# Kernel optimization log

Measured on AMD Instinct MI355X. Metric: run time of the kernel, lower is better.

The kernel has to match this reference:

```python
import jax, jax.numpy as jnp
import numpy as np
import math

B, CZ, L = 1, 128, 256
H, C = 4, 32  # num_heads, head dim
EPS = 1e-5


def _conv1x1(w, x):
    # w: (out, in), x: (b, in, i, j) -> (b, out, i, j)
    return jnp.einsum('oc,bcij->boij', w, x)


def setup_inputs() -> dict:
    key = jax.random.key(0)
    ks = jax.random.split(key, 8)
    s = 1.0 / math.sqrt(CZ)
    return {
        'pair_rep': jax.random.normal(ks[0], (B, CZ, L, L), jnp.float32),
        'ln_gamma': jnp.ones((CZ, L, L), jnp.float32),
        'ln_beta': jnp.zeros((CZ, L, L), jnp.float32),
        'w_q': jax.random.normal(ks[1], (H * C, CZ), jnp.float32) * s,
        'w_k': jax.random.normal(ks[2], (H * C, CZ), jnp.float32) * s,
        'w_v': jax.random.normal(ks[3], (H * C, CZ), jnp.float32) * s,
        'w_b': jax.random.normal(ks[4], (H, CZ), jnp.float32) * s,
        'w_g': jax.random.normal(ks[5], (H * C, CZ), jnp.float32) * s,
        'b_g': jnp.zeros((H * C,), jnp.float32),
        'w_rep': jax.random.normal(ks[6], (CZ, H * C), jnp.float32) * s,
        'b_rep': jnp.zeros((CZ,), jnp.float32),
    }


def reference(pair_rep, ln_gamma, ln_beta, w_q, w_k, w_v, w_b, w_g, b_g, w_rep, b_rep):
    # LayerNorm over (c_z, h, w) jointly, full-shape affine (torch LayerNorm([c_z,h,w]))
    mu = jnp.mean(pair_rep, axis=(1, 2, 3), keepdims=True)
    var = jnp.var(pair_rep, axis=(1, 2, 3), keepdims=True)
    x = (pair_rep - mu) * jax.lax.rsqrt(var + EPS) * ln_gamma[None] + ln_beta[None]

    # 1x1 conv projections; channels packed as (h c): channel = h*C + c
    q = _conv1x1(w_q, x).reshape(B, H, C, L, L)  # bhcij
    k = _conv1x1(w_k, x).reshape(B, H, C, L, L)
    v = _conv1x1(w_v, x).reshape(B, H, C, L, L)
    bias = _conv1x1(w_b, x)                       # (b, h, i, j) -> used as bias[b,h,j,k]
    g = jax.nn.sigmoid(_conv1x1(w_g, x) + b_g[None, :, None, None]).reshape(B, H, C, L, L)

    scale = 1.0 / math.sqrt(C)
    # scores[b,h,i,j,k] = scale * sum_c q[b,h,c,i,j] k[b,h,c,i,k] + bias[b,h,j,k]
    scores = scale * jnp.einsum('bhcij,bhcik->bhijk', q, k) + bias[:, :, None, :, :]
    a = jax.nn.softmax(scores, axis=-1)
    # o[b,h,c,i,j] = sum_k a[b,h,i,j,k] v[b,h,c,i,k]  (same math as the 6D broadcast-sum)
    o = g * jnp.einsum('bhijk,bhcik->bhcij', a, v)

    # output repacks channels as (c h): channel = c*H + h
    o = jnp.transpose(o, (0, 2, 1, 3, 4)).reshape(B, C * H, L, L)
    return _conv1x1(w_rep, o) + b_rep[None, :, None, None]
```

## Files before the change

kernel.cpp:

```cpp
#include <hip/hip_runtime.h>
#include <math.h>

#define L 256
#define CZ 128
#define NH 4
#define HD 32
#define P (L*L)
#define NTOT (CZ*P)
#define EPSV 1e-5f
#define SCALE 0.17677669529663687f

typedef unsigned short u16;
typedef _Float16 f16;
typedef __attribute__((ext_vector_type(8))) _Float16 f16x8;
typedef __attribute__((ext_vector_type(4))) _Float16 f16x4;
typedef __attribute__((ext_vector_type(4))) float    f32x4;

__device__ __forceinline__ float bu2f(u16 u){ return __uint_as_float(((unsigned)u) << 16); }
__device__ __forceinline__ u16 f2bu(float x){
  unsigned u = __float_as_uint(x);
  return (u16)((u + 0x7fffu + ((u >> 16) & 1u)) >> 16);
}

__device__ __forceinline__ float ldr(bool fp32, const void* p, size_t i){
  return fp32 ? ((const float*)p)[i] : bu2f(((const u16*)p)[i]);
}
__device__ __forceinline__ void str(bool fp32, void* p, size_t i, float v){
  if (fp32) ((float*)p)[i] = v; else ((u16*)p)[i] = f2bu(v);
}
template<bool FP32>
__device__ __forceinline__ float ldin(const void* p, size_t i){
  return FP32 ? ((const float*)p)[i] : bu2f(((const u16*)p)[i]);
}
template<bool FP32>
__device__ __forceinline__ void stout(void* p, size_t i, float v){
  if (FP32) ((float*)p)[i] = v; else ((u16*)p)[i] = f2bu(v);
}

__device__ __forceinline__ void glds16(const void* g, void* l){
  __builtin_amdgcn_global_load_lds((const __attribute__((address_space(1))) void*)g,
                                   (__attribute__((address_space(3))) void*)l, 16, 0, 0);
}

#define OFF_WQT   16
#define OFF_WKT   (OFF_WQT+16384)
#define OFF_WVT   (OFF_WKT+16384)
#define OFF_WGT   (OFF_WVT+16384)
#define OFF_WREPT (OFF_WGT+16384)
#define OFF_WBT   (OFF_WREPT+16384)
#define OFF_BGF   (OFF_WBT+512)
#define OFF_BREPF (OFF_BGF+128)
#define OFF_BIAS  (OFF_BREPF+128)
#define OFF_XN    344848
#define OFF_ATTO  (OFF_XN+4194304)
#define WS_NEED   (((size_t)OFF_ATTO + 4194304ull)*4ull)

#define GUARD(ws) if (((((const volatile int*)(ws))[2]) != 0) != FP32) return;
#define RFLAG(ws) (((const volatile int*)(ws))[2] != 0)

__global__ __launch_bounds__(256) void detect_dtype(const void* pair, int* flag){
  int t = threadIdx.x;
  const u16* u = (const u16*)pair;
  int big = 0;
  for (int k = t; k < 2048; k += 256){
    float av = fabsf(bu2f(u[k]));
    if (!(av < 1e4f)) big = 1;
  }
  __shared__ int sb[256];
  sb[t] = big; __syncthreads();
  for (int off = 128; off > 0; off >>= 1){
    if (t < off) sb[t] |= sb[t+off];
    __syncthreads();
  }
  if (t == 0) flag[2] = sb[0];
}

__global__ __launch_bounds__(256) void prep_w(const void* wq, const void* wk,
    const void* wv, const void* wg, const void* wrep, const void* wb,
    const void* bg, const void* brep, float* ws){
  bool fp32 = RFLAG(ws);
  int idx = blockIdx.x*256 + threadIdx.x;
  int oc = idx >> 7, cin = idx & 127;
  f16* wf = (f16*)(ws + OFF_WQT);
  wf[0*16384 + idx] = (f16)ldr(fp32, wq, idx);
  wf[1*16384 + idx] = (f16)ldr(fp32, wk, idx);
  wf[2*16384 + idx] = (f16)ldr(fp32, wv, idx);
  wf[3*16384 + idx] = (f16)ldr(fp32, wg, idx);
  float wr = ldr(fp32, wrep, idx);
  ws[OFF_WREPT + cin*128 + oc] = wr;
  ((f16*)(ws + OFF_WVT))[oc*128 + (cin&3)*32 + (cin>>2)] = (f16)wr;
  if (idx < 512){ int h = idx >> 7, ci = idx & 127; ws[OFF_WBT + ci*4 + h] = ldr(fp32, wb, idx); }
  if (idx < 128){ ws[OFF_BGF + idx] = ldr(fp32, bg, idx); ws[OFF_BREPF + idx] = ldr(fp32, brep, idx); }
}

__global__ __launch_bounds__(256) void ln_reduce(const void* __restrict__ pair, float* ws){
  bool fp32 = RFLAG(ws);
  int t = threadIdx.x;
  int g = blockIdx.x*256 + t;
  float s = 0.f, ss = 0.f;
  if (fp32){
    #pragma unroll
    for (int u = 0; u < 4; ++u){
      float4 v = ((const float4*)pair)[(size_t)u*524288 + g];
      s += v.x+v.y+v.z+v.w;
      ss += v.x*v.x + v.y*v.y + v.z*v.z + v.w*v.w;
    }
  } else {
    #pragma unroll
    for (int u = 0; u < 4; ++u){
      ushort4 v = ((const ushort4*)pair)[(size_t)u*524288 + g];
      float a = bu2f(v.x), b = bu2f(v.y), c = bu2f(v.z), d = bu2f(v.w);
      s += a+b+c+d; ss += a*a+b*b+c*c+d*d;
    }
  }
  __shared__ float sa[256], sb[256];
  sa[t] = s; sb[t] = ss;
  __syncthreads();
  for (int off = 128; off > 0; off >>= 1){
    if (t < off){ sa[t] += sa[t+off]; sb[t] += sb[t+off]; }
    __syncthreads();
  }
  if (t == 0){ atomicAdd(&ws[0], sa[0]); atomicAdd(&ws[1], sb[0]); }
}


__global__ __launch_bounds__(256) void xnorm(const void* __restrict__ pair,
    const void* __restrict__ gamma, const void* __restrict__ beta, float* __restrict__ ws){
  bool fp32 = RFLAG(ws);
  int a = blockIdx.x & 255, q = blockIdx.x >> 8;
  int t = threadIdx.x;
  int cq = t >> 6, b64 = t & 63, j4 = b64 << 2;
  float mu   = ws[0] * (1.0f/NTOT);
  float var  = ws[1] * (1.0f/NTOT) - mu*mu;
  float rstd = rsqrtf(var + EPSV);
  f16 hv[4][8];
  float pb[4][4];
  #pragma unroll
  for (int col = 0; col < 4; ++col)
    #pragma unroll
    for (int h = 0; h < 4; ++h) pb[col][h] = 0.f;
  #pragma unroll
  for (int ce = 0; ce < 8; ++ce){
    int c = q*32 + cq*8 + ce;
    size_t vi = (size_t)c*16384 + (size_t)a*64 + b64;
    float p0,p1,p2,p3, g0,g1,g2,g3, e0,e1,e2,e3;
    if (fp32){
      float4 pv = ((const float4*)pair)[vi];
      float4 gv = ((const float4*)gamma)[vi];
      float4 bv = ((const float4*)beta)[vi];
      p0=pv.x;p1=pv.y;p2=pv.z;p3=pv.w; g0=gv.x;g1=gv.y;g2=gv.z;g3=gv.w; e0=bv.x;e1=bv.y;e2=bv.z;e3=bv.w;
    } else {
      ushort4 pv = ((const ushort4*)pair)[vi];
      ushort4 gv = ((const ushort4*)gamma)[vi];
      ushort4 bv = ((const ushort4*)beta)[vi];
      p0=bu2f(pv.x);p1=bu2f(pv.y);p2=bu2f(pv.z);p3=bu2f(pv.w);
      g0=bu2f(gv.x);g1=bu2f(gv.y);g2=bu2f(gv.z);g3=bu2f(gv.w);
      e0=bu2f(bv.x);e1=bu2f(bv.y);e2=bu2f(bv.z);e3=bu2f(bv.w);
    }
    float x0 = (p0-mu)*rstd*g0 + e0;
    float x1 = (p1-mu)*rstd*g1 + e1;
    float x2 = (p2-mu)*rstd*g2 + e2;
    float x3 = (p3-mu)*rstd*g3 + e3;
    hv[0][ce] = (f16)x0; hv[1][ce] = (f16)x1; hv[2][ce] = (f16)x2; hv[3][ce] = (f16)x3;
    float4 w4 = *(const float4*)(ws + OFF_WBT + c*4);
    pb[0][0] = fmaf(w4.x, x0, pb[0][0]); pb[0][1] = fmaf(w4.y, x0, pb[0][1]);
    pb[0][2] = fmaf(w4.z, x0, pb[0][2]); pb[0][3] = fmaf(w4.w, x0, pb[0][3]);
    pb[1][0] = fmaf(w4.x, x1, pb[1][0]); pb[1][1] = fmaf(w4.y, x1, pb[1][1]);
    pb[1][2] = fmaf(w4.z, x1, pb[1][2]); pb[1][3] = fmaf(w4.w, x1, pb[1][3]);
    pb[2][0] = fmaf(w4.x, x2, pb[2][0]); pb[2][1] = fmaf(w4.y, x2, pb[2][1]);
    pb[2][2] = fmaf(w4.z, x2, pb[2][2]); pb[2][3] = fmaf(w4.w, x2, pb[2][3]);
    pb[3][0] = fmaf(w4.x, x3, pb[3][0]); pb[3][1] = fmaf(w4.y, x3, pb[3][1]);
    pb[3][2] = fmaf(w4.z, x3, pb[3][2]); pb[3][3] = fmaf(w4.w, x3, pb[3][3]);
  }
  char* xnb = (char*)ws + (size_t)OFF_XN*4;
  int cb = q*4 + cq;
  #pragma unroll
  for (int col = 0; col < 4; ++col){
    f16x8 v;
    #pragma unroll
    for (int ce = 0; ce < 8; ++ce) v[ce] = hv[col][ce];
    *(f16x8*)(xnb + ((((size_t)a*16 + cb)*256) + (j4+col))*16) = v;
  }
  __shared__ float sbb[4][64][16];
  #pragma unroll
  for (int col = 0; col < 4; ++col)
    #pragma unroll
    for (int h = 0; h < 4; ++h) sbb[cq][b64][h*4+col] = pb[col][h];
  __syncthreads();
  #pragma unroll
  for (int k = 0; k < 4; ++k){
    int lin = k*256 + t;
    int bb = lin >> 4, hc = lin & 15;
    float v = sbb[0][bb][hc] + sbb[1][bb][hc] + sbb[2][bb][hc] + sbb[3][bb][hc];
    int h = hc >> 2, col = hc & 3;
    atomicAdd(&ws[OFF_BIAS + h*P + a*256 + bb*4 + col], v - 1.0f);
  }
}

__global__ __launch_bounds__(256, 4) void attn_xn(float* __restrict__ ws){
  __shared__ __align__(16) char smem[32768];
  char* Ab = smem;
  char* Bb = smem + 16384;
  const int t = threadIdx.x;
  int bid = blockIdx.x;
  int sw = ((bid & 7) << 7) | (bid >> 3);
  const int h = sw >> 8, i = sw & 255;
  const int w = t >> 6, l = t & 63;
  const int l15 = l & 15, l4 = l >> 4;
  const char* xnb = (const char*)ws + (size_t)OFF_XN*4 + (size_t)i*65536;
  const f16* wf = (const f16*)(ws + OFF_WQT);

  auto stage = [&](int q){
    #pragma unroll
    for (int cbl = 0; cbl < 4; ++cbl){
      int jsrc = (w*64 + l) ^ cbl;
      const char* src = xnb + (size_t)((q*4 + cbl)*4096) + (size_t)jsrc*16;
      glds16(src, Ab + cbl*4096 + w*1024);
    }
  };

  f32x4 acc[2][4][2];
  auto projpass = [&](int pr0){
    #pragma unroll
    for (int pp = 0; pp < 2; ++pp)
      #pragma unroll
      for (int mj = 0; mj < 4; ++mj)
        #pragma unroll
        for (int nt = 0; nt < 2; ++nt) acc[pp][mj][nt] = f32x4{0.f,0.f,0.f,0.f};
    #pragma unroll
    for (int q = 0; q < 4; ++q){
      __syncthreads();
      f16x8 A[4];
      #pragma unroll
      for (int mj = 0; mj < 4; ++mj){
        int j = 64*w + 16*mj + l15;
        A[mj] = *(const f16x8*)(Ab + l4*4096 + ((j ^ l4)*16));
      }
      __syncthreads();
      if (q < 3) stage(q+1);
      #pragma unroll
      for (int pp = 0; pp < 2; ++pp){
        #pragma unroll
        for (int nt = 0; nt < 2; ++nt){
          int o = h*32 + nt*16 + l15;
          f16x8 Bf = *(const f16x8*)(wf + (pr0+pp)*16384 + o*128 + q*32 + 8*l4);
          #pragma unroll
          for (int mj = 0; mj < 4; ++mj)
            acc[pp][mj][nt] = __builtin_amdgcn_mfma_f32_16x16x32_f16(A[mj], Bf, acc[pp][mj][nt], 0, 0, 0);
        }
      }
    }
  };

  stage(0);
  projpass(0);
  __syncthreads();
  stage(0);
  #pragma unroll
  for (int mj = 0; mj < 4; ++mj){
    #pragma unroll
    for (int nt = 0; nt < 2; ++nt){
      int ob = 2*nt + (l15 >> 3), oe = l15 & 7;
      int kb4 = 64*w + 16*mj + 4*l4;
      #pragma unroll
      for (int r = 0; r < 4; ++r)
        *(f16*)(Bb + ((ob*4096 + (kb4+r)*16 + oe*2) ^ ((ob&3)<<4))) = (f16)acc[0][mj][nt][r];
    }
  }
  __syncthreads();
  f16x8 qa[4];
  #pragma unroll
  for (int mj = 0; mj < 4; ++mj){
    int j = 64*w + 16*mj + l15;
    qa[mj] = *(const f16x8*)(Bb + ((l4*4096 + j*16) ^ ((l4&3)<<4)));
  }
  __syncthreads();
  #pragma unroll
  for (int mj = 0; mj < 4; ++mj){
    #pragma unroll
    for (int nt = 0; nt < 2; ++nt){
      int ob = 2*nt + (l15 >> 3), oe = l15 & 7;
      int kb4 = 64*w + 16*mj + 4*l4;
      #pragma unroll
      for (int r = 0; r < 4; ++r)
        *(f16*)(Bb + ((ob*4096 + (kb4+r)*16 + oe*2) ^ ((ob&3)<<4))) = (f16)acc[1][mj][nt][r];
    }
  }

  projpass(2);
  f16x4 gsh[4][2];
  #pragma unroll
  for (int mj = 0; mj < 4; ++mj){
    #pragma unroll
    for (int nt = 0; nt < 2; ++nt){
      float bgv = ws[OFF_BGF + h*32 + nt*16 + l15];
      #pragma unroll
      for (int r = 0; r < 4; ++r){
        float z = acc[1][mj][nt][r] + bgv;
        gsh[mj][nt][r] = (f16)(1.0f/(1.0f + __expf(-z)));
      }
    }
  }
  __syncthreads();
  #pragma unroll
  for (int mj = 0; mj < 4; ++mj){
    #pragma unroll
    for (int nt = 0; nt < 2; ++nt){
      int c = nt*16 + l15;
      int kkq = 16*w + 4*mj + l4;
      f16x4 pv;
      #pragma unroll
      for (int r = 0; r < 4; ++r) pv[r] = (f16)acc[0][mj][nt][r];
      *(f16x4*)(Ab + kkq*256 + ((c*8) ^ (l4<<3))) = pv;
    }
  }
  __syncthreads();

  f32x4 oacc[4][2];
  #pragma unroll
  for (int mj = 0; mj < 4; ++mj)
    #pragma unroll
    for (int nt = 0; nt < 2; ++nt) oacc[mj][nt] = f32x4{0.f,0.f,0.f,0.f};
  float lp[4] = {0.f,0.f,0.f,0.f};
  const float* bias2 = ws + OFF_BIAS + (size_t)h*P;
  const f32x4 zz = {0.f,0.f,0.f,0.f};

  for (int kt = 0; kt < 8; ++kt){
    int kk0 = kt*32, kkq0 = kt*8;
    float4 bvv[4][2];
    #pragma unroll
    for (int mj = 0; mj < 4; ++mj){
      const float* bp = bias2 + (size_t)(64*w + 16*mj + l15)*256 + kk0 + 4*l4;
      bvv[mj][0] = *(const float4*)bp;
      bvv[mj][1] = *(const float4*)(bp + 16);
    }
    f16x8 kbf[2];
    #pragma unroll
    for (int tt = 0; tt < 2; ++tt)
      kbf[tt] = *(const f16x8*)(Bb + ((l4*4096 + (kk0+16*tt+l15)*16) ^ ((l4&3)<<4)));
    f16x4 vb[2][2];
    #pragma unroll
    for (int tt = 0; tt < 2; ++tt)
      #pragma unroll
      for (int nt = 0; nt < 2; ++nt)
        vb[tt][nt] = *(const f16x4*)(Ab + (kkq0+4*tt+l4)*256 + ((((l15+16*nt)*8)) ^ (l4<<3)));
    #pragma unroll
    for (int mj = 0; mj < 4; ++mj){
      #pragma unroll
      for (int tt = 0; tt < 2; ++tt){
        f32x4 s = __builtin_amdgcn_mfma_f32_16x16x32_f16(kbf[tt], qa[mj], zz, 0, 0, 0);
        float4 bv = bvv[mj][tt];
        f16x4 pa;
        {
          float e0 = __expf(fmaf(s[0], SCALE, bv.x));
          float e1 = __expf(fmaf(s[1], SCALE, bv.y));
          float e2 = __expf(fmaf(s[2], SCALE, bv.z));
          float e3 = __expf(fmaf(s[3], SCALE, bv.w));
          lp[mj] += (e0+e1)+(e2+e3);
          pa[0]=(f16)e0; pa[1]=(f16)e1; pa[2]=(f16)e2; pa[3]=(f16)e3;
        }
        #pragma unroll
        for (int nt = 0; nt < 2; ++nt)
          oacc[mj][nt] = __builtin_amdgcn_mfma_f32_16x16x16f16(pa, vb[tt][nt], oacc[mj][nt], 0, 0, 0);
      }
    }
  }

  float inv[4];
  #pragma unroll
  for (int mj = 0; mj < 4; ++mj){
    float v = lp[mj];
    v += __shfl_xor(v, 16);
    v += __shfl_xor(v, 32);
    inv[mj] = 1.0f / v;
  }
  __syncthreads();
  #pragma unroll
  for (int mj = 0; mj < 4; ++mj){
    #pragma unroll
    for (int r = 0; r < 4; ++r){
      float iv = __shfl(inv[mj], 20*l4 + r);
      int j = 64*w + 16*mj + 4*l4 + r;
      #pragma unroll
      for (int nt = 0; nt < 2; ++nt){
        int c = nt*16 + l15;
        float ov = oacc[mj][nt][r] * iv * (float)gsh[mj][nt][r];
        *(f16*)(Bb + c*512 + ((j*2) ^ ((c&7)<<4))) = (f16)ov;
      }
    }
  }
  __syncthreads();
  char* ao = (char*)ws + (size_t)OFF_ATTO*4 + (size_t)h*4194304 + ((size_t)i*256)*64;
  #pragma unroll
  for (int cb8 = 0; cb8 < 4; ++cb8){
    f16x8 v;
    #pragma unroll
    for (int e = 0; e < 8; ++e){
      int c = cb8*8 + e;
      v[e] = *(const f16*)(Bb + c*512 + ((t*2) ^ ((c&7)<<4)));
    }
    *(f16x8*)(ao + (size_t)t*64 + cb8*16) = v;
  }
}

__global__ __launch_bounds__(256, 4) void out_proj_mf(float* __restrict__ ws, void* __restrict__ outp){
  bool fp32 = RFLAG(ws);
  __shared__ __align__(16) char smem[32768];
  char* Ab = smem;
  char* Ob = smem + 16384;
  const int t = threadIdx.x;
  int bid = blockIdx.x;
  int sw2 = ((bid & 7) << 7) | (bid >> 3);
  const int oh = sw2 >> 8, i = sw2 & 255;
  const int w = t >> 6, l = t & 63;
  const int l15 = l & 15, l4 = l >> 4;
  const char* aob = (const char*)ws + (size_t)OFF_ATTO*4;
  const f16* w2 = (const f16*)(ws + OFF_WVT);

  auto stage = [&](int q){
    #pragma unroll
    for (int cbl = 0; cbl < 4; ++cbl){
      int jsrc = (w*64 + l) ^ cbl;
      const char* src = aob + (size_t)q*4194304 + ((size_t)i*256 + jsrc)*64 + cbl*16;
      glds16(src, Ab + cbl*4096 + w*1024);
    }
  };

  f32x4 acc[2][4];
  #pragma unroll
  for (int nt = 0; nt < 2; ++nt)
    #pragma unroll
    for (int mj = 0; mj < 4; ++mj) acc[nt][mj] = f32x4{0.f,0.f,0.f,0.f};

  stage(0);
  #pragma unroll
  for (int q = 0; q < 4; ++q){
    __syncthreads();
    f16x8 A[4];
    #pragma unroll
    for (int mj = 0; mj < 4; ++mj){
      int j = 64*w + 16*mj + l15;
      A[mj] = *(const f16x8*)(Ab + l4*4096 + ((j ^ l4)*16));
    }
    __syncthreads();
    if (q < 3) stage(q+1);
    #pragma unroll
    for (int nt = 0; nt < 2; ++nt){
      int oc = oh*32 + nt*16 + l15;
      f16x8 Bf = *(const f16x8*)(w2 + oc*128 + q*32 + 8*l4);
      #pragma unroll
      for (int mj = 0; mj < 4; ++mj)
        acc[nt][mj] = __builtin_amdgcn_mfma_f32_16x16x32_f16(A[mj], Bf, acc[nt][mj], 0, 0, 0);
    }
  }
  #pragma unroll
  for (int nt = 0; nt < 2; ++nt){
    __syncthreads();
    #pragma unroll
    for (int mj = 0; mj < 4; ++mj){
      #pragma unroll
      for (int r = 0; r < 4; ++r){
        int j = 64*w + 16*mj + 4*l4 + r;
        *(float*)(Ob + l15*1024 + ((j*4) ^ ((l15&7)<<4))) = acc[nt][mj][r];
      }
    }
    __syncthreads();
    #pragma unroll
    for (int o2 = 0; o2 < 16; ++o2){
      int oc = oh*32 + nt*16 + o2;
      float v = *(const float*)(Ob + o2*1024 + ((t*4) ^ ((o2&7)<<4)));
      str(fp32, outp, (size_t)oc*P + (size_t)i*L + t, v + ws[OFF_BREPF + oc]);
    }
  }
}


template<bool FP32>
__global__ __launch_bounds__(256) void bias_old(const void* __restrict__ pair,
    const void* __restrict__ gamma, const void* __restrict__ beta, float* __restrict__ ws){
  GUARD(ws);
  int a = blockIdx.x & 255, q = blockIdx.x >> 8, b = threadIdx.x;
  float mu   = ws[0] * (1.0f/NTOT);
  float var  = ws[1] * (1.0f/NTOT) - mu*mu;
  float rstd = rsqrtf(var + EPSV);
  float a0=0.f, a1=0.f, a2=0.f, a3=0.f;
  int c0 = q*32;
  for (int cc = 0; cc < 32; ++cc){
    int c = c0 + cc;
    size_t idx = (size_t)c*P + (size_t)a*L + b;
    float xv = (ldin<FP32>(pair,idx) - mu)*rstd*ldin<FP32>(gamma,idx) + ldin<FP32>(beta,idx);
    const float* w4 = ws + OFF_WBT + c*4;
    a0 = fmaf(w4[0], xv, a0); a1 = fmaf(w4[1], xv, a1);
    a2 = fmaf(w4[2], xv, a2); a3 = fmaf(w4[3], xv, a3);
  }
  atomicAdd(&ws[OFF_BIAS + 0*P + a*L + b], a0);
  atomicAdd(&ws[OFF_BIAS + 1*P + a*L + b], a1);
  atomicAdd(&ws[OFF_BIAS + 2*P + a*L + b], a2);
  atomicAdd(&ws[OFF_BIAS + 3*P + a*L + b], a3);
}

template<bool FP32>
__global__ __launch_bounds__(256, 2) void attn_old(const void* __restrict__ pair,
    const void* __restrict__ gamma, const void* __restrict__ beta,
    float* __restrict__ ws, void* __restrict__ outp){
  GUARD(ws);
  __shared__ __align__(16) char smem[65536];
  char* Ab  = smem;
  char* KTb = smem + 32768;
  char* V2b = smem + 49152;
  const int t = threadIdx.x;
  const int h = blockIdx.x >> 8, i = blockIdx.x & 255;
  const int w = t >> 6, l = t & 63;
  const int l15 = l & 15, l4 = l >> 4;
  const float mu   = ws[0] * (1.0f/NTOT);
  const float var  = ws[1] * (1.0f/NTOT) - mu*mu;
  const float rstd = rsqrtf(var + EPSV);
  const f16* wf = (const f16*)(ws + OFF_WQT);
  f32x4 acc[4][4][2];
  #pragma unroll
  for (int pr=0;pr<4;++pr)
    #pragma unroll
    for(int mj=0;mj<4;++mj)
      #pragma unroll
      for(int nt=0;nt<2;++nt) acc[pr][mj][nt] = f32x4{0.f,0.f,0.f,0.f};
  for (int half = 0; half < 2; ++half){
    #pragma unroll
    for (int cb = 0; cb < 8; ++cb){
      int cc0 = cb*8;
      f16x8 hv;
      #pragma unroll
      for (int e = 0; e < 8; ++e){
        size_t idx = (size_t)(half*64 + cc0 + e)*P + (size_t)i*L + t;
        float xv = (ldin<FP32>(pair,idx) - mu)*rstd*ldin<FP32>(gamma,idx) + ldin<FP32>(beta,idx);
        hv[e] = (f16)xv;
      }
      *(f16x8*)(Ab + t*128 + ((cc0*2) ^ ((t&7)<<4))) = hv;
    }
    __syncthreads();
    #pragma unroll
    for (int ksl = 0; ksl < 2; ++ksl){
      int cin0 = half*64 + ksl*32;
      f16x8 A[4];
      #pragma unroll
      for (int mj = 0; mj < 4; ++mj){
        int j = 64*w + 16*mj + l15;
        A[mj] = *(const f16x8*)(Ab + j*128 + (((ksl*32 + 8*l4)*2) ^ ((j&7)<<4)));
      }
      #pragma unroll
      for (int pr = 0; pr < 4; ++pr){
        #pragma unroll
        for (int nt = 0; nt < 2; ++nt){
          int o = h*32 + nt*16 + l15;
          f16x8 Bf = *(const f16x8*)(wf + pr*16384 + o*128 + cin0 + 8*l4);
          #pragma unroll
          for (int mj = 0; mj < 4; ++mj)
            acc[pr][mj][nt] = __builtin_amdgcn_mfma_f32_16x16x32_f16(A[mj], Bf, acc[pr][mj][nt], 0, 0, 0);
        }
      }
    }
    __syncthreads();
  }
  f32x4 gs[4][2];
  #pragma unroll
  for (int mj = 0; mj < 4; ++mj){
    #pragma unroll
    for (int nt = 0; nt < 2; ++nt){
      float bgv = ws[OFF_BGF + h*32 + nt*16 + l15];
      #pragma unroll
      for (int r = 0; r < 4; ++r){
        float z = acc[3][mj][nt][r] + bgv;
        gs[mj][nt][r] = 1.0f/(1.0f + __expf(-z));
      }
    }
  }
  #pragma unroll
  for (int mj = 0; mj < 4; ++mj){
    #pragma unroll
    for (int nt = 0; nt < 2; ++nt){
      int o = nt*16 + l15;
      int kb4 = 64*w + 16*mj + 4*l4;
      f16x4 pv;
      #pragma unroll
      for (int r = 0; r < 4; ++r){
        int j = kb4 + r;
        *(f16*)(Ab  + j*64 + ((o*2) ^ ((j&3)<<4))) = (f16)acc[0][mj][nt][r];
        *(f16*)(KTb + j*64 + ((o*2) ^ ((j&3)<<4))) = (f16)acc[1][mj][nt][r];
        pv[r] = (f16)acc[2][mj][nt][r];
      }
      *(f16x4*)(V2b + o*512 + ((kb4*2) ^ ((o&7)<<4))) = pv;
    }
  }
  __syncthreads();
  f16x8 qa[4];
  #pragma unroll
  for (int mj = 0; mj < 4; ++mj){
    int j = 64*w + 16*mj + l15;
    qa[mj] = *(const f16x8*)(Ab + j*64 + ((16*l4) ^ ((j&3)<<4)));
  }
  __syncthreads();
  f32x4 oacc[4][2];
  #pragma unroll
  for (int mj=0;mj<4;++mj)
    #pragma unroll
    for(int nt=0;nt<2;++nt) oacc[mj][nt] = f32x4{0.f,0.f,0.f,0.f};
  float lp[16];
  #pragma unroll
  for (int u = 0; u < 16; ++u) lp[u] = 0.f;
  const float* bias2 = ws + OFF_BIAS + (size_t)h*P;
  const f32x4 zz = {0.f,0.f,0.f,0.f};
  for (int kt = 0; kt < 4; ++kt){
    int kk0 = kt*64;
    #pragma unroll
    for (int nk = 0; nk < 4; ++nk){
      int kkr = kk0 + nk*16 + l15;
      f16x8 kbf = *(const f16x8*)(KTb + kkr*64 + ((16*l4) ^ ((kkr&3)<<4)));
      #pragma unroll
      for (int mj = 0; mj < 4; ++mj){
        f32x4 s = __builtin_amdgcn_mfma_f32_16x16x32_f16(qa[mj], kbf, zz, 0, 0, 0);
        #pragma unroll
        for (int r = 0; r < 4; ++r){
          int j = 64*w + 16*mj + 4*l4 + r;
          float bv = bias2[(size_t)j*L + kkr] - 4.0f;
          float e = __expf(fmaf(s[r], SCALE, bv));
          lp[mj*4+r] += e;
          *(f16*)(Ab + j*128 + (((nk*16+l15)*2) ^ ((j&7)<<4))) = (f16)e;
        }
      }
    }
    __syncthreads();
    #pragma unroll
    for (int ks2 = 0; ks2 < 2; ++ks2){
      f16x8 vb[2];
      #pragma unroll
      for (int nt = 0; nt < 2; ++nt){
        int c = nt*16 + l15;
        vb[nt] = *(const f16x8*)(V2b + c*512 + (((kk0 + ks2*32 + 8*l4)*2) ^ ((c&7)<<4)));
      }
      #pragma unroll
      for (int mj = 0; mj < 4; ++mj){
        int j = 64*w + 16*mj + l15;
        f16x8 pa = *(const f16x8*)(Ab + j*128 + (((ks2*32 + 8*l4)*2) ^ ((j&7)<<4)));
        #pragma unroll
        for (int nt = 0; nt < 2; ++nt)
          oacc[mj][nt] = __builtin_amdgcn_mfma_f32_16x16x32_f16(pa, vb[nt], oacc[mj][nt], 0, 0, 0);
      }
    }
  }
  __syncthreads();
  #pragma unroll
  for (int u = 0; u < 16; ++u){
    float v = lp[u];
    v += __shfl_xor(v, 1);
    v += __shfl_xor(v, 2);
    v += __shfl_xor(v, 4);
    v += __shfl_xor(v, 8);
    lp[u] = 1.0f / v;
  }
  #pragma unroll
  for (int mj = 0; mj < 4; ++mj){
    #pragma unroll
    for (int nt = 0; nt < 2; ++nt){
      int c = nt*16 + l15;
      #pragma unroll
      for (int r = 0; r < 4; ++r){
        int j = 64*w + 16*mj + 4*l4 + r;
        float ov = oacc[mj][nt][r] * lp[mj*4+r] * gs[mj][nt][r];
        *(float*)(Ab + c*1024 + ((j*4) ^ ((c&7)<<4))) = ov;
      }
    }
  }
  __syncthreads();
  #pragma unroll
  for (int c = 0; c < 32; ++c){
    float v = *(const float*)(Ab + c*1024 + ((t*4) ^ ((c&7)<<4)));
    stout<FP32>(outp, (size_t)(c*NH + h)*P + (size_t)i*L + t, v);
  }
}

template<bool FP32>
__global__ __launch_bounds__(256) void out_proj_old(float* __restrict__ ws, void* __restrict__ outp){
  GUARD(ws);
  __shared__ float gos[CZ*65];
  int blk = blockIdx.x;
  int i = blk >> 2, jb = (blk & 3) << 6;
  int t = threadIdx.x;
  for (int u = 0; u < 32; ++u){
    int lin = u*256 + t;
    int m = lin >> 6, p = lin & 63;
    gos[m*65 + p] = ldin<FP32>(outp, (size_t)m*P + (size_t)i*L + jb + p);
  }
  __syncthreads();
  int p = t & 63, w4 = t >> 6;
  int woc = w4*32;
  float acc[32];
  #pragma unroll
  for (int o = 0; o < 32; ++o) acc[o] = 0.f;
  for (int cin = 0; cin < CZ; ++cin){
    float xv = gos[cin*65 + p];
    const float* wrow = ws + OFF_WREPT + cin*128 + woc;
    #pragma unroll
    for (int o = 0; o < 32; ++o) acc[o] = fmaf(wrow[o], xv, acc[o]);
  }
  #pragma unroll
  for (int o = 0; o < 32; ++o){
    int oc = woc + o;
    stout<FP32>(outp, (size_t)oc*P + (size_t)i*L + jb + p, acc[o] + ws[OFF_BREPF + oc]);
  }
}

extern "C" void kernel_launch(void* const* d_in, const int* in_sizes, int n_in,
                              void* d_out, int out_size, void* d_ws, size_t ws_size,
                              hipStream_t stream) {
  (void)in_sizes; (void)n_in; (void)out_size;
  const void* pair  = d_in[0];
  const void* gamma = d_in[1];
  const void* beta  = d_in[2];
  const void* wq    = d_in[3];
  const void* wk    = d_in[4];
  const void* wv    = d_in[5];
  const void* wb    = d_in[6];
  const void* wg    = d_in[7];
  const void* bg    = d_in[8];
  const void* wrep  = d_in[9];
  const void* brep  = d_in[10];
  float* ws = (float*)d_ws;
  bool big = ws_size >= WS_NEED;

  hipMemsetAsync(d_ws, 0, 16, stream);
  hipMemsetAsync((char*)d_ws + (size_t)OFF_BIAS*4, 0, (size_t)NH*P*4, stream);
  detect_dtype<<<1, 256, 0, stream>>>(pair, (int*)d_ws);

  prep_w   <<<64,   256, 0, stream>>>(wq, wk, wv, wg, wrep, wb, bg, brep, ws);
  ln_reduce<<<2048, 256, 0, stream>>>(pair, ws);

  if (big){
    xnorm      <<<1024, 256, 0, stream>>>(pair, gamma, beta, ws);
    attn_xn    <<<1024, 256, 0, stream>>>(ws);
    out_proj_mf<<<1024, 256, 0, stream>>>(ws, d_out);
  } else {
    bias_old<false>    <<<1024, 256, 0, stream>>>(pair, gamma, beta, ws);
    bias_old<true>     <<<1024, 256, 0, stream>>>(pair, gamma, beta, ws);
    attn_old<false>    <<<1024, 256, 0, stream>>>(pair, gamma, beta, ws, d_out);
    attn_old<true>     <<<1024, 256, 0, stream>>>(pair, gamma, beta, ws, d_out);
    out_proj_old<false><<<1024, 256, 0, stream>>>(ws, d_out);
    out_proj_old<true> <<<1024, 256, 0, stream>>>(ws, d_out);
  }
}
```

Measured before the change: 317.4 us.

## Fuse setup launches, remap attention block order, vectorize attention output stores

```diff
diff --git a/kernel.cpp b/kernel.cpp
--- a/kernel.cpp
+++ b/kernel.cpp
@@ -58,8 +58,12 @@
 #define GUARD(ws) if (((((const volatile int*)(ws))[2]) != 0) != FP32) return;
 #define RFLAG(ws) (((const volatile int*)(ws))[2] != 0)
 
-__global__ __launch_bounds__(256) void detect_dtype(const void* pair, int* flag){
-  int t = threadIdx.x;
+__global__ __launch_bounds__(256) void detect_zero(const void* pair, float* ws){
+  int b = blockIdx.x, t = threadIdx.x;
+  if (b > 0){
+    ((float4*)(ws + OFF_BIAS))[(size_t)(b-1)*256 + t] = float4{0.f,0.f,0.f,0.f};
+    return;
+  }
   const u16* u = (const u16*)pair;
   int big = 0;
   for (int k = t; k < 2048; k += 256){
@@ -72,31 +76,29 @@
     if (t < off) sb[t] |= sb[t+off];
     __syncthreads();
   }
-  if (t == 0) flag[2] = sb[0];
-}
-
-__global__ __launch_bounds__(256) void prep_w(const void* wq, const void* wk,
-    const void* wv, const void* wg, const void* wrep, const void* wb,
-    const void* bg, const void* brep, float* ws){
+  if (t == 0){ ((int*)ws)[2] = sb[0]; ws[0] = 0.f; ws[1] = 0.f; }
+}
+
+__global__ __launch_bounds__(256) void lnprep(const void* __restrict__ pair,
+    const void* wq, const void* wk, const void* wv, const void* wg,
+    const void* wrep, const void* wb, const void* bg, const void* brep, float* ws){
   bool fp32 = RFLAG(ws);
-  int idx = blockIdx.x*256 + threadIdx.x;
-  int oc = idx >> 7, cin = idx & 127;
-  f16* wf = (f16*)(ws + OFF_WQT);
-  wf[0*16384 + idx] = (f16)ldr(fp32, wq, idx);
-  wf[1*16384 + idx] = (f16)ldr(fp32, wk, idx);
-  wf[2*16384 + idx] = (f16)ldr(fp32, wv, idx);
-  wf[3*16384 + idx] = (f16)ldr(fp32, wg, idx);
-  float wr = ldr(fp32, wrep, idx);
-  ws[OFF_WREPT + cin*128 + oc] = wr;
-  ((f16*)(ws + OFF_WVT))[oc*128 + (cin&3)*32 + (cin>>2)] = (f16)wr;
-  if (idx < 512){ int h = idx >> 7, ci = idx & 127; ws[OFF_WBT + ci*4 + h] = ldr(fp32, wb, idx); }
-  if (idx < 128){ ws[OFF_BGF + idx] = ldr(fp32, bg, idx); ws[OFF_BREPF + idx] = ldr(fp32, brep, idx); }
-}
-
-__global__ __launch_bounds__(256) void ln_reduce(const void* __restrict__ pair, float* ws){
-  bool fp32 = RFLAG(ws);
-  int t = threadIdx.x;
-  int g = blockIdx.x*256 + t;
+  int b = blockIdx.x, t = threadIdx.x;
+  if (b < 64){
+    int idx = b*256 + t;
+    int oc = idx >> 7, cin = idx & 127;
+    f16* wf = (f16*)(ws + OFF_WQT);
+    wf[0*16384 + idx] = (f16)ldr(fp32, wq, idx);
+    wf[1*16384 + idx] = (f16)ldr(fp32, wk, idx);
+    wf[2*16384 + idx] = (f16)ldr(fp32, wv, idx);
+    wf[3*16384 + idx] = (f16)ldr(fp32, wg, idx);
+    float wr = ldr(fp32, wrep, idx);
+    ws[OFF_WREPT + cin*128 + oc] = wr;
+    ((f16*)(ws + OFF_WVT))[oc*128 + (cin&3)*32 + (cin>>2)] = (f16)wr;
+    if (idx < 512){ int h = idx >> 7, ci = idx & 127; ws[OFF_WBT + ci*4 + h] = ldr(fp32, wb, idx); }
+    if (idx < 128){ ws[OFF_BGF + idx] = ldr(fp32, bg, idx); ws[OFF_BREPF + idx] = ldr(fp32, brep, idx); }
+  }
+  int g = b*256 + t;
   float s = 0.f, ss = 0.f;
   if (fp32){
     #pragma unroll
@@ -109,18 +111,18 @@
     #pragma unroll
     for (int u = 0; u < 4; ++u){
       ushort4 v = ((const ushort4*)pair)[(size_t)u*524288 + g];
-      float a = bu2f(v.x), b = bu2f(v.y), c = bu2f(v.z), d = bu2f(v.w);
-      s += a+b+c+d; ss += a*a+b*b+c*c+d*d;
-    }
-  }
-  __shared__ float sa[256], sb[256];
-  sa[t] = s; sb[t] = ss;
+      float a = bu2f(v.x), bq = bu2f(v.y), c = bu2f(v.z), d = bu2f(v.w);
+      s += a+bq+c+d; ss += a*a+bq*bq+c*c+d*d;
+    }
+  }
+  __shared__ float sa[256], sbf[256];
+  sa[t] = s; sbf[t] = ss;
   __syncthreads();
   for (int off = 128; off > 0; off >>= 1){
-    if (t < off){ sa[t] += sa[t+off]; sb[t] += sb[t+off]; }
-    __syncthreads();
-  }
-  if (t == 0){ atomicAdd(&ws[0], sa[0]); atomicAdd(&ws[1], sb[0]); }
+    if (t < off){ sa[t] += sa[t+off]; sbf[t] += sbf[t+off]; }
+    __syncthreads();
+  }
+  if (t == 0){ atomicAdd(&ws[0], sa[0]); atomicAdd(&ws[1], sbf[0]); }
 }
 
 
@@ -203,8 +205,8 @@
   char* Bb = smem + 16384;
   const int t = threadIdx.x;
   int bid = blockIdx.x;
-  int sw = ((bid & 7) << 7) | (bid >> 3);
-  const int h = sw >> 8, i = sw & 255;
+  int W = (bid & 7)*128 + (bid >> 3);
+  const int i = W >> 2, h = W & 3;
   const int w = t >> 6, l = t & 63;
   const int l15 = l & 15, l4 = l >> 4;
   const char* xnb = (const char*)ws + (size_t)OFF_XN*4 + (size_t)i*65536;
@@ -381,25 +383,23 @@
     for (int r = 0; r < 4; ++r){
       float iv = __shfl(inv[mj], 20*l4 + r);
       int j = 64*w + 16*mj + 4*l4 + r;
+      int swz = ((j>>2)&3)<<4;
       #pragma unroll
       for (int nt = 0; nt < 2; ++nt){
         int c = nt*16 + l15;
         float ov = oacc[mj][nt][r] * iv * (float)gsh[mj][nt][r];
-        *(f16*)(Bb + c*512 + ((j*2) ^ ((c&7)<<4))) = (f16)ov;
+        *(f16*)(Bb + ((j*64 + c*2) ^ swz)) = (f16)ov;
       }
     }
   }
   __syncthreads();
   char* ao = (char*)ws + (size_t)OFF_ATTO*4 + (size_t)h*4194304 + ((size_t)i*256)*64;
   #pragma unroll
-  for (int cb8 = 0; cb8 < 4; ++cb8){
-    f16x8 v;
-    #pragma unroll
-    for (int e = 0; e < 8; ++e){
-      int c = cb8*8 + e;
-      v[e] = *(const f16*)(Bb + c*512 + ((t*2) ^ ((c&7)<<4)));
-    }
-    *(f16x8*)(ao + (size_t)t*64 + cb8*16) = v;
+  for (int u = 0; u < 4; ++u){
+    int lin = u*256 + t;
+    int j = lin >> 2;
+    f16x8 v = *(const f16x8*)(Bb + ((j*64 + (lin&3)*16) ^ (((j>>2)&3)<<4)));
+    *(f16x8*)(ao + (size_t)lin*16) = v;
   }
 }
 
@@ -410,8 +410,8 @@
   char* Ob = smem + 16384;
   const int t = threadIdx.x;
   int bid = blockIdx.x;
-  int sw2 = ((bid & 7) << 7) | (bid >> 3);
-  const int oh = sw2 >> 8, i = sw2 & 255;
+  int W = (bid & 7)*128 + (bid >> 3);
+  const int i = W >> 2, oh = W & 3;
   const int w = t >> 6, l = t & 63;
   const int l15 = l & 15, l4 = l >> 4;
   const char* aob = (const char*)ws + (size_t)OFF_ATTO*4;
@@ -726,12 +726,8 @@
   float* ws = (float*)d_ws;
   bool big = ws_size >= WS_NEED;
 
-  hipMemsetAsync(d_ws, 0, 16, stream);
-  hipMemsetAsync((char*)d_ws + (size_t)OFF_BIAS*4, 0, (size_t)NH*P*4, stream);
-  detect_dtype<<<1, 256, 0, stream>>>(pair, (int*)d_ws);
-
-  prep_w   <<<64,   256, 0, stream>>>(wq, wk, wv, wg, wrep, wb, bg, brep, ws);
-  ln_reduce<<<2048, 256, 0, stream>>>(pair, ws);
+  detect_zero<<<257,  256, 0, stream>>>(pair, ws);
+  lnprep     <<<2048, 256, 0, stream>>>(pair, wq, wk, wv, wg, wrep, wb, bg, brep, ws);
 
   if (big){
     xnorm      <<<1024, 256, 0, stream>>>(pair, gamma, beta, ws);
```

Measured after the change: 302.5 us. 1.05x faster.
